# Performance work log

Hardware: AMD Instinct MI355X
Metric: run time of the kernel (lower is better)

Reference implementation:

```python
import jax, jax.numpy as jnp
import numpy as np

NUM_HEADS = 8
KERNEL = 7  # odd, dilation = 1


def _neighbor_indices(n, k):
    # NATTEN semantics: window start clamped so the kxk window stays inside [0, n)
    r = k // 2
    starts = jnp.clip(jnp.arange(n) - r, 0, n - k)  # [n]
    return starts[:, None] + jnp.arange(k)[None, :]  # [n, k]


def setup_inputs() -> dict:
    key = jax.random.key(0)
    k1, k2, k3, k4 = jax.random.split(key, 4)
    B, H, W, C = 2, 56, 56, 256
    return {
        "x": jax.random.normal(k1, (B, H, W, C), dtype=jnp.float32),
        "w_qk": jax.random.normal(k2, (2 * C, C), dtype=jnp.float32) * 0.02,
        "w_v": jax.random.normal(k3, (C, C), dtype=jnp.float32) * 0.02,
        "w_proj": jax.random.normal(k4, (C, C), dtype=jnp.float32) * 0.02,
        "b_proj": jnp.zeros((C,), dtype=jnp.float32),
    }


def reference(x, w_qk, w_v, w_proj, b_proj):
    B, H, W, C = x.shape
    NH, K = NUM_HEADS, KERNEL
    HD = C // NH
    scale = HD ** -0.5

    # qk / v projections (torch Linear: y = x @ W.T)
    qk = (x @ w_qk.T).reshape(B, H, W, 2, NH, HD)
    q = jnp.moveaxis(qk[:, :, :, 0], 3, 1) * scale  # [B, NH, H, W, HD]
    k = jnp.moveaxis(qk[:, :, :, 1], 3, 1)          # [B, NH, H, W, HD]
    v = jnp.moveaxis((x @ w_v.T).reshape(B, H, W, NH, HD), 3, 1)  # [B, NH, H, W, HD]

    idx_h = _neighbor_indices(H, K)  # [H, K]
    idx_w = _neighbor_indices(W, K)  # [W, K]
    ih = idx_h[:, None, :, None]  # [H, 1, K, 1]
    iw = idx_w[None, :, None, :]  # [1, W, 1, K]

    # Gather per-pixel neighborhoods: [B, NH, H, W, K, K, HD]
    k_nb = k[:, :, ih, iw, :]
    v_nb = v[:, :, ih, iw, :]

    # windowed QK^T -> [B, NH, H, W, K*K]
    attn = jnp.einsum('bnijf,bnijpqf->bnijpq', q, k_nb).reshape(B, NH, H, W, K * K)
    attn = jax.nn.softmax(attn, axis=-1)

    # windowed AV -> [B, NH, H, W, HD]
    out = jnp.einsum('bnijk,bnijkf->bnijf', attn, v_nb.reshape(B, NH, H, W, K * K, HD))

    out = jnp.moveaxis(out, 1, 3).reshape(B, H, W, C)
    out = out @ w_proj.T + b_proj
    return out, attn
```

## Files before the change

### kernel.cpp

```cpp
#include <hip/hip_runtime.h>
#include <math.h>

#define Bb   2
#define Hh   56
#define Ww   56
#define Cc   256
#define NHh  8
#define HDd  32
#define KK   7
#define HWsz (Hh*Ww)
#define Mtot (Bb*Hh*Ww)

typedef __bf16 bf16x8 __attribute__((ext_vector_type(8)));
typedef __bf16 bf16x4 __attribute__((ext_vector_type(4)));
typedef float  f32x4  __attribute__((ext_vector_type(4)));

__global__ __launch_bounds__(256) void gemm_bf16(
    const float* __restrict__ A, const float* __restrict__ W0,
    const float* __restrict__ W1, float* __restrict__ Cout,
    int Kdim, int N, int n_split, int scale_below, float scale,
    const float* __restrict__ bias)
{
    __shared__ __bf16 As[4096];
    __shared__ __bf16 Bs[4096];

    const int tid = threadIdx.x;
    const int m0  = blockIdx.y * 64;
    const int n0  = blockIdx.x * 64;

    const int mm = tid >> 2;
    const int q  = tid & 3;
    const float* arow = A + (size_t)(m0 + mm) * Kdim + q * 16;
    const int n_idx = n0 + mm;
    const float* brow = (n_idx < n_split ? W0 + (size_t)n_idx * Kdim
                                         : W1 + (size_t)(n_idx - n_split) * Kdim) + q * 16;

    const int ks_st  = q >> 1;
    const int sub_st = mm >> 4;
    const int row_st = mm & 15;
    const int c0_st  = (q & 1) * 2;
    const int blk_st = ks_st * 4 + sub_st;
    const int off0 = blk_st * 512 + row_st * 32 + ((c0_st ^ (row_st & 3)) * 8);
    const int off1 = blk_st * 512 + row_st * 32 + (((c0_st + 1) ^ (row_st & 3)) * 8);

    const int w    = tid >> 6;
    const int lane = tid & 63;
    const int fr_row = lane & 15;
    const int fr_c   = lane >> 4;
    const int fr_off = fr_row * 32 + ((fr_c ^ (fr_row & 3)) * 8);

    f32x4 acc[4] = {};

    for (int k0 = 0; k0 < Kdim; k0 += 64) {
        float4 a0 = *(const float4*)(arow + k0);
        float4 a1 = *(const float4*)(arow + k0 + 4);
        float4 a2 = *(const float4*)(arow + k0 + 8);
        float4 a3 = *(const float4*)(arow + k0 + 12);
        float4 b0 = *(const float4*)(brow + k0);
        float4 b1 = *(const float4*)(brow + k0 + 4);
        float4 b2 = *(const float4*)(brow + k0 + 8);
        float4 b3 = *(const float4*)(brow + k0 + 12);
        __syncthreads();
        bf16x8 av0 = { (__bf16)a0.x, (__bf16)a0.y, (__bf16)a0.z, (__bf16)a0.w,
                       (__bf16)a1.x, (__bf16)a1.y, (__bf16)a1.z, (__bf16)a1.w };
        bf16x8 av1 = { (__bf16)a2.x, (__bf16)a2.y, (__bf16)a2.z, (__bf16)a2.w,
                       (__bf16)a3.x, (__bf16)a3.y, (__bf16)a3.z, (__bf16)a3.w };
        bf16x8 bv0 = { (__bf16)b0.x, (__bf16)b0.y, (__bf16)b0.z, (__bf16)b0.w,
                       (__bf16)b1.x, (__bf16)b1.y, (__bf16)b1.z, (__bf16)b1.w };
        bf16x8 bv1 = { (__bf16)b2.x, (__bf16)b2.y, (__bf16)b2.z, (__bf16)b2.w,
                       (__bf16)b3.x, (__bf16)b3.y, (__bf16)b3.z, (__bf16)b3.w };
        *(bf16x8*)&As[off0] = av0;
        *(bf16x8*)&As[off1] = av1;
        *(bf16x8*)&Bs[off0] = bv0;
        *(bf16x8*)&Bs[off1] = bv1;
        __syncthreads();
        #pragma unroll
        for (int ks = 0; ks < 2; ++ks) {
            bf16x8 af = *(const bf16x8*)&As[(ks * 4 + w) * 512 + fr_off];
            #pragma unroll
            for (int n = 0; n < 4; ++n) {
                bf16x8 bfr = *(const bf16x8*)&Bs[(ks * 4 + n) * 512 + fr_off];
                acc[n] = __builtin_amdgcn_mfma_f32_16x16x32_bf16(af, bfr, acc[n], 0, 0, 0);
            }
        }
    }

    #pragma unroll
    for (int n = 0; n < 4; ++n) {
        const int gcol = n0 + n * 16 + fr_row;
        const float sc_ = (gcol < scale_below) ? scale : 1.f;
        const float bs_ = bias ? bias[gcol] : 0.f;
        #pragma unroll
        for (int r = 0; r < 4; ++r) {
            const int grow = m0 + w * 16 + fr_c * 4 + r;
            Cout[(size_t)grow * N + gcol] = acc[n][r] * sc_ + bs_;
        }
    }
}

__global__ __launch_bounds__(256, 5) void nattn_84(
    const float* __restrict__ qkv, float* __restrict__ attn_out,
    float* __restrict__ attn_glob)
{
    __shared__ __align__(16) __bf16 Ks[140 * 40];
    __shared__ float Ss[32 * 49];

    const int bx   = blockIdx.x;
    const int head = bx & 7;
    int t = bx >> 3;
    const int tj = t % 14; t /= 14;
    const int ti = t % 7;
    const int b  = t / 7;
    const int tid = threadIdx.x;

    int base_h = ti * 8 - 3; if (base_h < 0) base_h = 0; if (base_h > Hh - 14) base_h = Hh - 14;
    int base_w = tj * 4 - 3; if (base_w < 0) base_w = 0; if (base_w > Ww - 10) base_w = Ww - 10;

    const int pixb = b * HWsz;
    const int hoff = head * 32;

    #pragma unroll
    for (int it = 0; it < 3; ++it) {
        const int idx = tid + it * 256;
        if (idx < 560) {
            const int p = idx >> 2, c = idx & 3;
            const int pix = pixb + (base_h + p / 10) * Ww + base_w + p % 10;
            const float* kp = &qkv[(size_t)pix * 768 + 256 + hoff + c * 8];
            float4 k0 = *(const float4*)kp;
            float4 k1 = *(const float4*)(kp + 4);
            bf16x8 kb = { (__bf16)k0.x, (__bf16)k0.y, (__bf16)k0.z, (__bf16)k0.w,
                          (__bf16)k1.x, (__bf16)k1.y, (__bf16)k1.z, (__bf16)k1.w };
            *(bf16x8*)&Ks[p * 40 + c * 8] = kb;
        }
    }

    const int q  = tid >> 3;
    const int r  = tid & 7;
    const int qi = ti * 8 + (q >> 2);
    const int qj = tj * 4 + (q & 3);

    float qreg[32];
    {
        const float* qp = &qkv[(size_t)(pixb + qi * Ww + qj) * 768 + hoff];
        #pragma unroll
        for (int c = 0; c < 8; ++c) {
            float4 qv = *(const float4*)(qp + c * 4);
            qreg[c * 4 + 0] = qv.x; qreg[c * 4 + 1] = qv.y;
            qreg[c * 4 + 2] = qv.z; qreg[c * 4 + 3] = qv.w;
        }
    }

    float4 vreg[6];
    #pragma unroll
    for (int it = 0; it < 3; ++it) {
        const int idx = tid + it * 256;
        if (idx < 560) {
            const int p = idx >> 2, c = idx & 3;
            const int pix = pixb + (base_h + p / 10) * Ww + base_w + p % 10;
            const float* vp = &qkv[(size_t)pix * 768 + 512 + hoff + c * 8];
            vreg[it * 2]     = *(const float4*)vp;
            vreg[it * 2 + 1] = *(const float4*)(vp + 4);
        }
    }
    __syncthreads();

    int ih0 = qi - 3; if (ih0 < 0) ih0 = 0; if (ih0 > Hh - 7) ih0 = Hh - 7;
    int iw0 = qj - 3; if (iw0 < 0) iw0 = 0; if (iw0 > Ww - 7) iw0 = Ww - 7;
    const int lh0 = ih0 - base_h, lw0 = iw0 - base_w;

    float sc[7];
    float mx = -1e30f;
    #pragma unroll
    for (int tt = 0; tt < 7; ++tt) {
        const int k = r + 8 * tt;
        if (k < 49) {
            const int krow = (lh0 + k / 7) * 10 + lw0 + k % 7;
            const __bf16* kp = &Ks[krow * 40];
            float acc = 0.f;
            #pragma unroll
            for (int c = 0; c < 4; ++c) {
                bf16x8 kv = *(const bf16x8*)(kp + c * 8);
                #pragma unroll
                for (int j = 0; j < 8; ++j)
                    acc += qreg[c * 8 + j] * (float)kv[j];
            }
            sc[tt] = acc;
            mx = fmaxf(mx, acc);
        }
    }
    mx = fmaxf(mx, __shfl_xor(mx, 1));
    mx = fmaxf(mx, __shfl_xor(mx, 2));
    mx = fmaxf(mx, __shfl_xor(mx, 4));
    float sum = 0.f;
    #pragma unroll
    for (int tt = 0; tt < 7; ++tt) {
        const int k = r + 8 * tt;
        if (k < 49) { sc[tt] = __expf(sc[tt] - mx); sum += sc[tt]; }
    }
    sum += __shfl_xor(sum, 1);
    sum += __shfl_xor(sum, 2);
    sum += __shfl_xor(sum, 4);
    const float inv = 1.f / sum;
    #pragma unroll
    for (int tt = 0; tt < 7; ++tt) {
        const int k = r + 8 * tt;
        if (k < 49) Ss[q * 49 + k] = sc[tt] * inv;
    }
    __syncthreads();

    #pragma unroll
    for (int it = 0; it < 3; ++it) {
        const int idx = tid + it * 256;
        if (idx < 560) {
            const int p = idx >> 2, c = idx & 3;
            const float4 v0 = vreg[it * 2], v1 = vreg[it * 2 + 1];
            bf16x8 vb = { (__bf16)v0.x, (__bf16)v0.y, (__bf16)v0.z, (__bf16)v0.w,
                          (__bf16)v1.x, (__bf16)v1.y, (__bf16)v1.z, (__bf16)v1.w };
            *(bf16x8*)&Ks[p * 40 + c * 8] = vb;
        }
    }
    const size_t agbase = (size_t)(b * NHh + head) * HWsz;
    for (int idx = tid; idx < 32 * 49; idx += 256) {
        const int qq = idx / 49, k = idx - qq * 49;
        attn_glob[(agbase + (ti * 8 + (qq >> 2)) * Ww + tj * 4 + (qq & 3)) * 49 + k]
            = Ss[qq * 49 + k];
    }
    __syncthreads();

    const int rc  = r & 3;
    const int par = r >> 2;
    float a[8] = {};
    #pragma unroll
    for (int tt = 0; tt < 25; ++tt) {
        const int k = par + 2 * tt;
        if (k < 49) {
            const float pr = Ss[q * 49 + k];
            const int vrow = (lh0 + k / 7) * 10 + lw0 + k % 7;
            bf16x8 v8 = *(const bf16x8*)&Ks[vrow * 40 + rc * 8];
            #pragma unroll
            for (int j = 0; j < 8; ++j)
                a[j] += pr * (float)v8[j];
        }
    }
    #pragma unroll
    for (int j = 0; j < 8; ++j) a[j] += __shfl_xor(a[j], 4);

    float4 o;
    o.x = a[par * 4 + 0]; o.y = a[par * 4 + 1];
    o.z = a[par * 4 + 2]; o.w = a[par * 4 + 3];
    *(float4*)(attn_out + (size_t)(pixb + qi * Ww + qj) * 256 + hoff + rc * 8 + par * 4) = o;
}

extern "C" void kernel_launch(void* const* d_in, const int* in_sizes, int n_in,
                              void* d_out, int out_size, void* d_ws, size_t ws_size,
                              hipStream_t stream)
{
    const float* x      = (const float*)d_in[0];
    const float* w_qk   = (const float*)d_in[1];
    const float* w_v    = (const float*)d_in[2];
    const float* w_proj = (const float*)d_in[3];
    const float* b_proj = (const float*)d_in[4];

    float* out       = (float*)d_out;
    float* attn_glob = out + (size_t)Mtot * Cc;

    float* qkv_ws  = (float*)d_ws;
    float* attn_ws = qkv_ws + (size_t)Mtot * 768;

    const float scale = 0.17677669529663687f;

    gemm_bf16<<<dim3(768 / 64, Mtot / 64), 256, 0, stream>>>(
        x, w_qk, w_v, qkv_ws, Cc, 768, 512, 256, scale, nullptr);

    nattn_84<<<Bb * 7 * 14 * NHh, 256, 0, stream>>>(qkv_ws, attn_ws, attn_glob);

    gemm_bf16<<<dim3(256 / 64, Mtot / 64), 256, 0, stream>>>(
        attn_ws, w_proj, w_proj, out, Cc, Cc, 1 << 30, 0, 1.f, b_proj);
}
```

Before: 113.2 us.

## Store K/V intermediates and attention output in bf16 to cut memory traffic

The QKV GEMM now writes Q as fp32 and K/V as bf16, packed into one interleaved per-pixel buffer. The attention kernel loads K/V directly as bf16 vectors and writes its per-head output as bf16. A new projection GEMM reads that bf16 activation directly. The aim is to halve the intermediate traffic and drop the in-kernel conversions, at the cost of rounding V and the attention output to bf16 earlier than before.

```diff
diff --git a/kernel.cpp b/kernel.cpp
--- a/kernel.cpp
+++ b/kernel.cpp
@@ -15,15 +15,15 @@
 typedef __bf16 bf16x4 __attribute__((ext_vector_type(4)));
 typedef float  f32x4  __attribute__((ext_vector_type(4)));
 
-__global__ __launch_bounds__(256) void gemm_bf16(
+__global__ __launch_bounds__(256) void gemm_qkv(
     const float* __restrict__ A, const float* __restrict__ W0,
-    const float* __restrict__ W1, float* __restrict__ Cout,
-    int Kdim, int N, int n_split, int scale_below, float scale,
-    const float* __restrict__ bias)
+    const float* __restrict__ W1, float* __restrict__ OutF,
+    __bf16* __restrict__ OutB, float scale)
 {
     __shared__ __bf16 As[4096];
     __shared__ __bf16 Bs[4096];
 
+    const int Kdim = 256, n_split = 512;
     const int tid = threadIdx.x;
     const int m0  = blockIdx.y * 64;
     const int n0  = blockIdx.x * 64;
@@ -85,25 +85,111 @@
         }
     }
 
+    if (n0 < 256) {
+        #pragma unroll
+        for (int n = 0; n < 4; ++n) {
+            const int gcol = n0 + n * 16 + fr_row;
+            #pragma unroll
+            for (int r = 0; r < 4; ++r) {
+                const int grow = m0 + w * 16 + fr_c * 4 + r;
+                OutF[(size_t)grow * 512 + gcol] = acc[n][r] * scale;
+            }
+        }
+    } else {
+        #pragma unroll
+        for (int n = 0; n < 4; ++n) {
+            const int gcol = n0 + n * 16 + fr_row;
+            #pragma unroll
+            for (int r = 0; r < 4; ++r) {
+                const int grow = m0 + w * 16 + fr_c * 4 + r;
+                OutB[(size_t)grow * 1024 + 512 + (gcol - 256)] = (__bf16)acc[n][r];
+            }
+        }
+    }
+}
+
+__global__ __launch_bounds__(256) void gemm_a16(
+    const __bf16* __restrict__ A, const float* __restrict__ W,
+    float* __restrict__ Cout, const float* __restrict__ bias)
+{
+    __shared__ __bf16 As[4096];
+    __shared__ __bf16 Bs[4096];
+
+    const int Kdim = 256, N = 256;
+    const int tid = threadIdx.x;
+    const int m0  = blockIdx.y * 64;
+    const int n0  = blockIdx.x * 64;
+
+    const int mm = tid >> 2;
+    const int q  = tid & 3;
+    const __bf16* arow = A + (size_t)(m0 + mm) * Kdim + q * 16;
+    const float*  brow = W + (size_t)(n0 + mm) * Kdim + q * 16;
+
+    const int ks_st  = q >> 1;
+    const int sub_st = mm >> 4;
+    const int row_st = mm & 15;
+    const int c0_st  = (q & 1) * 2;
+    const int blk_st = ks_st * 4 + sub_st;
+    const int off0 = blk_st * 512 + row_st * 32 + ((c0_st ^ (row_st & 3)) * 8);
+    const int off1 = blk_st * 512 + row_st * 32 + (((c0_st + 1) ^ (row_st & 3)) * 8);
+
+    const int w    = tid >> 6;
+    const int lane = tid & 63;
+    const int fr_row = lane & 15;
+    const int fr_c   = lane >> 4;
+    const int fr_off = fr_row * 32 + ((fr_c ^ (fr_row & 3)) * 8);
+
+    f32x4 acc[4] = {};
+
+    for (int k0 = 0; k0 < Kdim; k0 += 64) {
+        bf16x8 av0 = *(const bf16x8*)(arow + k0);
+        bf16x8 av1 = *(const bf16x8*)(arow + k0 + 8);
+        float4 b0 = *(const float4*)(brow + k0);
+        float4 b1 = *(const float4*)(brow + k0 + 4);
+        float4 b2 = *(const float4*)(brow + k0 + 8);
+        float4 b3 = *(const float4*)(brow + k0 + 12);
+        __syncthreads();
+        bf16x8 bv0 = { (__bf16)b0.x, (__bf16)b0.y, (__bf16)b0.z, (__bf16)b0.w,
+                       (__bf16)b1.x, (__bf16)b1.y, (__bf16)b1.z, (__bf16)b1.w };
+        bf16x8 bv1 = { (__bf16)b2.x, (__bf16)b2.y, (__bf16)b2.z, (__bf16)b2.w,
+                       (__bf16)b3.x, (__bf16)b3.y, (__bf16)b3.z, (__bf16)b3.w };
+        *(bf16x8*)&As[off0] = av0;
+        *(bf16x8*)&As[off1] = av1;
+        *(bf16x8*)&Bs[off0] = bv0;
+        *(bf16x8*)&Bs[off1] = bv1;
+        __syncthreads();
+        #pragma unroll
+        for (int ks = 0; ks < 2; ++ks) {
+            bf16x8 af = *(const bf16x8*)&As[(ks * 4 + w) * 512 + fr_off];
+            #pragma unroll
+            for (int n = 0; n < 4; ++n) {
+                bf16x8 bfr = *(const bf16x8*)&Bs[(ks * 4 + n) * 512 + fr_off];
+                acc[n] = __builtin_amdgcn_mfma_f32_16x16x32_bf16(af, bfr, acc[n], 0, 0, 0);
+            }
+        }
+    }
+
     #pragma unroll
     for (int n = 0; n < 4; ++n) {
         const int gcol = n0 + n * 16 + fr_row;
-        const float sc_ = (gcol < scale_below) ? scale : 1.f;
-        const float bs_ = bias ? bias[gcol] : 0.f;
+        const float bs_ = bias[gcol];
         #pragma unroll
         for (int r = 0; r < 4; ++r) {
             const int grow = m0 + w * 16 + fr_c * 4 + r;
-            Cout[(size_t)grow * N + gcol] = acc[n][r] * sc_ + bs_;
+            Cout[(size_t)grow * N + gcol] = acc[n][r] + bs_;
         }
     }
 }
 
 __global__ __launch_bounds__(256, 5) void nattn_84(
-    const float* __restrict__ qkv, float* __restrict__ attn_out,
+    const float* __restrict__ qkv, __bf16* __restrict__ attn_out,
     float* __restrict__ attn_glob)
 {
     __shared__ __align__(16) __bf16 Ks[140 * 40];
     __shared__ float Ss[32 * 49];
+
+    const float*  qf = qkv;
+    const __bf16* qb = (const __bf16*)qkv;
 
     const int bx   = blockIdx.x;
     const int head = bx & 7;
@@ -125,12 +211,8 @@
         if (idx < 560) {
             const int p = idx >> 2, c = idx & 3;
             const int pix = pixb + (base_h + p / 10) * Ww + base_w + p % 10;
-            const float* kp = &qkv[(size_t)pix * 768 + 256 + hoff + c * 8];
-            float4 k0 = *(const float4*)kp;
-            float4 k1 = *(const float4*)(kp + 4);
-            bf16x8 kb = { (__bf16)k0.x, (__bf16)k0.y, (__bf16)k0.z, (__bf16)k0.w,
-                          (__bf16)k1.x, (__bf16)k1.y, (__bf16)k1.z, (__bf16)k1.w };
-            *(bf16x8*)&Ks[p * 40 + c * 8] = kb;
+            *(bf16x8*)&Ks[p * 40 + c * 8] =
+                *(const bf16x8*)&qb[(size_t)pix * 1024 + 512 + hoff + c * 8];
         }
     }
 
@@ -141,7 +223,7 @@
 
     float qreg[32];
     {
-        const float* qp = &qkv[(size_t)(pixb + qi * Ww + qj) * 768 + hoff];
+        const float* qp = &qf[(size_t)(pixb + qi * Ww + qj) * 512 + hoff];
         #pragma unroll
         for (int c = 0; c < 8; ++c) {
             float4 qv = *(const float4*)(qp + c * 4);
@@ -150,16 +232,14 @@
         }
     }
 
-    float4 vreg[6];
+    bf16x8 vreg[3];
     #pragma unroll
     for (int it = 0; it < 3; ++it) {
         const int idx = tid + it * 256;
         if (idx < 560) {
             const int p = idx >> 2, c = idx & 3;
             const int pix = pixb + (base_h + p / 10) * Ww + base_w + p % 10;
-            const float* vp = &qkv[(size_t)pix * 768 + 512 + hoff + c * 8];
-            vreg[it * 2]     = *(const float4*)vp;
-            vreg[it * 2 + 1] = *(const float4*)(vp + 4);
+            vreg[it] = *(const bf16x8*)&qb[(size_t)pix * 1024 + 768 + hoff + c * 8];
         }
     }
     __syncthreads();
@@ -213,10 +293,7 @@
         const int idx = tid + it * 256;
         if (idx < 560) {
             const int p = idx >> 2, c = idx & 3;
-            const float4 v0 = vreg[it * 2], v1 = vreg[it * 2 + 1];
-            bf16x8 vb = { (__bf16)v0.x, (__bf16)v0.y, (__bf16)v0.z, (__bf16)v0.w,
-                          (__bf16)v1.x, (__bf16)v1.y, (__bf16)v1.z, (__bf16)v1.w };
-            *(bf16x8*)&Ks[p * 40 + c * 8] = vb;
+            *(bf16x8*)&Ks[p * 40 + c * 8] = vreg[it];
         }
     }
     const size_t agbase = (size_t)(b * NHh + head) * HWsz;
@@ -245,10 +322,9 @@
     #pragma unroll
     for (int j = 0; j < 8; ++j) a[j] += __shfl_xor(a[j], 4);
 
-    float4 o;
-    o.x = a[par * 4 + 0]; o.y = a[par * 4 + 1];
-    o.z = a[par * 4 + 2]; o.w = a[par * 4 + 3];
-    *(float4*)(attn_out + (size_t)(pixb + qi * Ww + qj) * 256 + hoff + rc * 8 + par * 4) = o;
+    bf16x4 o = { (__bf16)a[par * 4 + 0], (__bf16)a[par * 4 + 1],
+                 (__bf16)a[par * 4 + 2], (__bf16)a[par * 4 + 3] };
+    *(bf16x4*)(attn_out + (size_t)(pixb + qi * Ww + qj) * 256 + hoff + rc * 8 + par * 4) = o;
 }
 
 extern "C" void kernel_launch(void* const* d_in, const int* in_sizes, int n_in,
@@ -264,16 +340,16 @@
     float* out       = (float*)d_out;
     float* attn_glob = out + (size_t)Mtot * Cc;
 
-    float* qkv_ws  = (float*)d_ws;
-    float* attn_ws = qkv_ws + (size_t)Mtot * 768;
+    float*  qkv_ws  = (float*)d_ws;
+    __bf16* attn_ws = (__bf16*)(qkv_ws + (size_t)Mtot * 512);
 
     const float scale = 0.17677669529663687f;
 
-    gemm_bf16<<<dim3(768 / 64, Mtot / 64), 256, 0, stream>>>(
-        x, w_qk, w_v, qkv_ws, Cc, 768, 512, 256, scale, nullptr);
+    gemm_qkv<<<dim3(768 / 64, Mtot / 64), 256, 0, stream>>>(
+        x, w_qk, w_v, qkv_ws, (__bf16*)qkv_ws, scale);
 
     nattn_84<<<Bb * 7 * 14 * NHh, 256, 0, stream>>>(qkv_ws, attn_ws, attn_glob);
 
-    gemm_bf16<<<dim3(256 / 64, Mtot / 64), 256, 0, stream>>>(
-        attn_ws, w_proj, w_proj, out, Cc, Cc, 1 << 30, 0, 1.f, b_proj);
+    gemm_a16<<<dim3(256 / 64, Mtot / 64), 256, 0, stream>>>(
+        attn_ws, w_proj, out, b_proj);
 }
```

After: 109.1 us. 1.04x faster.
